# Optimization experiments

Measured on AMD Instinct MI355X. Metric: run time of the kernel, lower is better.

The kernel has to match this reference:

```python
import jax, jax.numpy as jnp
import numpy as np

B, T, D, H, O, E = 2, 2048, 1024, 4096, 1024, 8


def setup_inputs() -> dict:
    key = jax.random.key(0)
    ks = jax.random.split(key, 8)
    s = lambda fan_in: 1.0 / np.sqrt(fan_in)
    return {
        "x": jax.random.normal(ks[0], (B, T, D), dtype=jnp.float32),
        "Wg": jax.random.uniform(ks[1], (D, E), minval=-s(D), maxval=s(D)),
        "bg": jax.random.uniform(ks[2], (E,), minval=-s(D), maxval=s(D)),
        "W1": jax.random.uniform(ks[3], (E, D, H), minval=-s(D), maxval=s(D)),
        "b1": jax.random.uniform(ks[4], (E, H), minval=-s(D), maxval=s(D)),
        "W2": jax.random.uniform(ks[5], (E, H, O), minval=-s(H), maxval=s(H)),
        "b2": jax.random.uniform(ks[6], (E, O), minval=-s(H), maxval=s(H)),
        "num_experts_per_tok": 2,
    }


def reference(x, Wg, bg, W1, b1, W2, b2, num_experts_per_tok):
    # gating: softmax over experts  [B,T,E]
    scores = jax.nn.softmax(jnp.einsum('btd,de->bte', x, Wg) + bg, axis=-1)
    # top-k mask (scatter of ones at topk indices)
    _, idx = jax.lax.top_k(scores, num_experts_per_tok)          # [B,T,k]
    mask = jax.nn.one_hot(idx, E, dtype=scores.dtype).sum(axis=-2)  # [B,T,E]
    gated = scores * mask
    # F.normalize(p=1): divide by L1 norm clamped to eps
    gated = gated / jnp.maximum(jnp.sum(jnp.abs(gated), axis=-1, keepdims=True), 1e-12)
    # all experts run on all tokens (naive MoE)
    hidden = jax.nn.relu(jnp.einsum('btd,edh->beth', x, W1) + b1[None, :, None, :])  # [B,E,T,H]
    expert_out = jnp.einsum('beth,eho->beto', hidden, W2) + b2[None, :, None, :]     # [B,E,T,O]
    # combine: einsum('bte,bteo->bto') with expert_outputs transposed(1,2)
    return jnp.einsum('bte,beto->bto', gated, expert_out)
```

## Files before the change

### kernel.cpp

```cpp
#include <hip/hip_runtime.h>
#include <hip/hip_bf16.h>
#include <cstdio>

#define NT_TOK 4096
#define D_DIM  1024
#define H_DIM  4096
#define O_DIM  1024
#define E_NUM  8
#define PAIRS  8192
#define WI_SLOTS 72
#define BK 64
#define G1_BLOCKS (32 * WI_SLOTS)
#define G2_BLOCKS (8 * WI_SLOTS)
#define TW1_BLOCKS (E_NUM * 1024)
#define TW2_BLOCKS (E_NUM * 1024)

typedef short bf16x8 __attribute__((ext_vector_type(8)));
typedef float f32x4  __attribute__((ext_vector_type(4)));

__device__ __forceinline__ unsigned short bfr(float f){
  unsigned u = __float_as_uint(f);
  unsigned r = (u + 0x7FFFu + ((u >> 16) & 1u)) >> 16;
  return (unsigned short)r;
}

__device__ __forceinline__ void gload_lds16(const void* g, void* l){
  __builtin_amdgcn_global_load_lds((const __attribute__((address_space(1))) unsigned int*)g,
                                   (__attribute__((address_space(3))) unsigned int*)l,
                                   16, 0, 0);
}

__device__ __forceinline__ void transpose_tile(const float* __restrict__ in,
                                               unsigned short* __restrict__ out,
                                               int R, int C, int bx, int by, int bz,
                                               char* smem){
  float (*t)[65] = (float(*)[65])smem;
  long long base = (long long)bz * R * C;
  int c0 = bx * 64, r0 = by * 64;
  int tid = threadIdx.x;
  int rr = tid >> 4;
  int cc = (tid & 15) * 4;
  #pragma unroll
  for (int i = 0; i < 4; i++){
    int r = rr + i * 16;
    float4 v = *(const float4*)&in[base + (long long)(r0 + r) * C + c0 + cc];
    t[r][cc] = v.x; t[r][cc+1] = v.y; t[r][cc+2] = v.z; t[r][cc+3] = v.w;
  }
  __syncthreads();
  #pragma unroll
  for (int i = 0; i < 4; i++){
    int oc = rr + i * 16;
    unsigned int lo = (unsigned int)bfr(t[cc][oc])   | ((unsigned int)bfr(t[cc+1][oc]) << 16);
    unsigned int hi = (unsigned int)bfr(t[cc+2][oc]) | ((unsigned int)bfr(t[cc+3][oc]) << 16);
    *(uint2*)&out[base + (long long)(c0 + oc) * R + r0 + cc] = make_uint2(lo, hi);
  }
}

__global__ __launch_bounds__(256) void gate_w1t_kernel(const float* __restrict__ x,
                                                       const float* __restrict__ Wg,
                                                       const float* __restrict__ bg,
                                                       const float* __restrict__ W1,
                                                       unsigned short* __restrict__ xb,
                                                       unsigned short* __restrict__ W1t,
                                                       int*   __restrict__ pe,
                                                       float* __restrict__ pw,
                                                       int*   __restrict__ chist){
  __shared__ __align__(16) char smem[16640];
  int bid = blockIdx.x;
  if (bid >= NT_TOK/4){
    int tb = bid - NT_TOK/4;
    int e = tb >> 10, t = tb & 1023;
    transpose_tile(W1, W1t, D_DIM, H_DIM, t & 63, t >> 6, e, smem);
    return;
  }
  int wid = threadIdx.x >> 6, lane = threadIdx.x & 63;
  int t = bid * 4 + wid;
  const float* xr = x + (long long)t * D_DIM;
  unsigned short* xo = xb + (long long)t * D_DIM;
  float acc[E_NUM];
  #pragma unroll
  for (int e = 0; e < E_NUM; e++) acc[e] = 0.f;
  for (int d = lane; d < D_DIM; d += 64){
    float xv = xr[d];
    xo[d] = bfr(xv);
    const float* wr = Wg + d * E_NUM;
    #pragma unroll
    for (int e = 0; e < E_NUM; e++) acc[e] += xv * wr[e];
  }
  #pragma unroll
  for (int off = 32; off; off >>= 1)
    #pragma unroll
    for (int e = 0; e < E_NUM; e++) acc[e] += __shfl_xor(acc[e], off);
  if (lane == 0){
    float l[E_NUM];
    float m = -1e30f;
    #pragma unroll
    for (int e = 0; e < E_NUM; e++){ l[e] = acc[e] + bg[e]; m = fmaxf(m, l[e]); }
    float ex[E_NUM];
    #pragma unroll
    for (int e = 0; e < E_NUM; e++) ex[e] = expf(l[e] - m);
    int e0 = 0;
    #pragma unroll
    for (int e = 1; e < E_NUM; e++) if (ex[e] > ex[e0]) e0 = e;
    int e1 = -1;
    for (int e = 0; e < E_NUM; e++){ if (e == e0) continue; if (e1 < 0 || ex[e] > ex[e1]) e1 = e; }
    float s = ex[e0] + ex[e1];
    pe[2*t]   = e0;  pw[2*t]   = ex[e0] / s;
    pe[2*t+1] = e1;  pw[2*t+1] = ex[e1] / s;
    int chunk = (2*t) >> 8;
    atomicAdd(&chist[chunk * E_NUM + e0], 1);
    atomicAdd(&chist[chunk * E_NUM + e1], 1);
  }
}

__global__ __launch_bounds__(256) void scatter_kernel(const int* __restrict__ pe,
                                                      const int* __restrict__ chunk_hist,
                                                      int* __restrict__ cnt,
                                                      int* __restrict__ offs,
                                                      int* __restrict__ row_pair,
                                                      int* __restrict__ wi){
  __shared__ int hist[32][E_NUM];
  __shared__ int pref[32][E_NUM];
  __shared__ int total[E_NUM];
  __shared__ int off_s[E_NUM + 1];
  __shared__ unsigned char ex[PAIRS];
  int tid = threadIdx.x;
  for (int i = tid; i < PAIRS; i += 256) ex[i] = (unsigned char)pe[i];
  { int c = tid >> 3, e = tid & 7; hist[c][e] = chunk_hist[tid]; }
  __syncthreads();
  if (tid < E_NUM){
    int s = 0;
    for (int c = 0; c < 32; c++){ pref[c][tid] = s; s += hist[c][tid]; }
    total[tid] = s;
  }
  __syncthreads();
  if (tid == 0){
    int s = 0;
    for (int e = 0; e < E_NUM; e++){ off_s[e] = s; s += total[e]; }
    off_s[E_NUM] = s;
    int idx = 0;
    for (int e = 0; e < E_NUM; e++){
      int mts = (total[e] + 127) >> 7;
      for (int m = 0; m < mts; m++) wi[idx++] = (e << 8) | m;
    }
    for (; idx < WI_SLOTS; idx++) wi[idx] = -1;
  }
  __syncthreads();
  if (tid < E_NUM){ cnt[tid] = total[tid]; offs[tid] = off_s[tid]; }
  int c = tid >> 3, e = tid & 7;
  int base = off_s[e] + pref[c][e];
  int local = 0;
  for (int i = 0; i < 256; i++){
    int p = c * 256 + i;
    if (ex[p] == (unsigned char)e){
      row_pair[base + local] = p;
      local++;
    }
  }
}

__global__ __launch_bounds__(256, 3) void gemm1_w2t_kernel(const unsigned short* __restrict__ xb,
                                                           const unsigned short* __restrict__ W1t,
                                                           const float* __restrict__ W2,
                                                           unsigned short* __restrict__ W2t,
                                                           const float* __restrict__ b1,
                                                           const int* __restrict__ row_pair,
                                                           const int* __restrict__ cnt,
                                                           const int* __restrict__ offs,
                                                           const int* __restrict__ wi,
                                                           unsigned short* __restrict__ hidden){
  __shared__ __align__(16) char smem[32768];
  int bid = blockIdx.x;
  if (bid >= G1_BLOCKS){
    int tb = bid - G1_BLOCKS;
    int e = tb >> 10, t = tb & 1023;
    transpose_tile(W2, W2t, H_DIM, O_DIM, t & 15, t >> 4, e, smem);
    return;
  }
  int nt = bid & 31, slot = bid >> 5;
  int w = wi[slot];
  if (w < 0) return;
  int e = w >> 8, mt = w & 255;
  int count = cnt[e];
  int m0 = mt * 128;
  int seg = offs[e];
  int valid = count - m0;
  int n0 = nt * 128;

  unsigned short* As = (unsigned short*)smem;
  unsigned short* Bs = (unsigned short*)(smem + 16384);

  int tid = threadIdx.x;
  int wv = tid >> 6, lane = tid & 63;
  int wr = wv >> 1, wc = wv & 1;
  int lo = lane & 15, hi = lane >> 4;
  int l3 = lane >> 3;
  int srcel = ((lane & 7) ^ l3) << 3;

  const unsigned short* w1e = W1t + (long long)e * H_DIM * D_DIM;

  const unsigned short* pa[4];
  const unsigned short* pb[4];
  #pragma unroll
  for (int h = 0; h < 4; h++){
    int r = h * 32 + wv * 8 + l3;
    int pos = seg + m0 + r; if (pos > PAIRS - 1) pos = PAIRS - 1;
    int token = row_pair[pos] >> 1;
    pa[h] = xb + (long long)token * D_DIM + srcel;
    pb[h] = w1e + (long long)(n0 + r) * D_DIM + srcel;
  }

  f32x4 acc[4][4] = {};
  for (int kt = 0; kt < D_DIM / BK; ++kt){
    #pragma unroll
    for (int h = 0; h < 4; h++){
      gload_lds16(pa[h], &As[(h*32 + wv*8) * BK]);  pa[h] += BK;
      gload_lds16(pb[h], &Bs[(h*32 + wv*8) * BK]);  pb[h] += BK;
    }
    __syncthreads();
    bf16x8 aq[4][2], bq[4][2];
    #pragma unroll
    for (int n = 0; n < 4; n++)
      #pragma unroll
      for (int ks = 0; ks < 2; ks++){
        int br = wc*64 + n*16 + lo;
        bq[n][ks] = *(const bf16x8*)&Bs[br*BK + ((ks*32 + hi*8) ^ ((br & 7) << 3))];
      }
    #pragma unroll
    for (int m = 0; m < 4; m++)
      #pragma unroll
      for (int ks = 0; ks < 2; ks++){
        int ar = wr*64 + m*16 + lo;
        aq[m][ks] = *(const bf16x8*)&As[ar*BK + ((ks*32 + hi*8) ^ ((ar & 7) << 3))];
      }
    #pragma unroll
    for (int m = 0; m < 4; m++)
      #pragma unroll
      for (int n = 0; n < 4; n++)
        #pragma unroll
        for (int ks = 0; ks < 2; ks++)
          acc[m][n] = __builtin_amdgcn_mfma_f32_16x16x32_bf16(aq[m][ks], bq[n][ks], acc[m][n], 0, 0, 0);
    __syncthreads();
  }

  const float* b1e = b1 + (long long)e * H_DIM;
  #pragma unroll
  for (int n = 0; n < 4; n++){
    int col = n0 + wc*64 + n*16 + lo;
    float bias = b1e[col];
    #pragma unroll
    for (int m = 0; m < 4; m++)
      #pragma unroll
      for (int j = 0; j < 4; j++){
        int rl = wr*64 + m*16 + hi*4 + j;
        if (rl < valid){
          float v = acc[m][n][j] + bias;
          v = v > 0.f ? v : 0.f;
          hidden[(long long)(seg + m0 + rl) * H_DIM + col] = bfr(v);
        }
      }
  }
}

__global__ __launch_bounds__(256, 3) void gemm2_kernel(const unsigned short* __restrict__ hidden,
                                                       const unsigned short* __restrict__ W2t,
                                                       const float* __restrict__ b2,
                                                       const int* __restrict__ row_pair,
                                                       const int* __restrict__ cnt,
                                                       const int* __restrict__ offs,
                                                       const int* __restrict__ wi,
                                                       float* __restrict__ y){
  int bid = blockIdx.x;
  int fp = (bid & 7) * (G2_BLOCKS / 8) + (bid >> 3);
  int nt = fp & 7, slot = fp >> 3;
  int w = wi[slot];
  if (w < 0) return;
  int e = w >> 8, mt = w & 255;
  int count = cnt[e];
  int m0 = mt * 128;
  int seg = offs[e];
  int valid = count - m0;
  int n0 = nt * 128;

  __shared__ unsigned short As[128 * BK];
  __shared__ unsigned short Bs[128 * BK];

  int tid = threadIdx.x;
  int wv = tid >> 6, lane = tid & 63;
  int wr = wv >> 1, wc = wv & 1;
  int lo = lane & 15, hi = lane >> 4;
  int l3 = lane >> 3;
  int srcel = ((lane & 7) ^ l3) << 3;

  const unsigned short* w2e = W2t + (long long)e * O_DIM * H_DIM;

  const unsigned short* pa[4];
  const unsigned short* pb[4];
  #pragma unroll
  for (int h = 0; h < 4; h++){
    int r = h * 32 + wv * 8 + l3;
    long long pos = seg + m0 + r; if (pos > PAIRS - 1) pos = PAIRS - 1;
    pa[h] = hidden + pos * H_DIM + srcel;
    pb[h] = w2e + (long long)(n0 + r) * H_DIM + srcel;
  }

  f32x4 acc[4][4] = {};
  for (int kt = 0; kt < H_DIM / BK; ++kt){
    #pragma unroll
    for (int h = 0; h < 4; h++){
      gload_lds16(pa[h], &As[(h*32 + wv*8) * BK]);  pa[h] += BK;
      gload_lds16(pb[h], &Bs[(h*32 + wv*8) * BK]);  pb[h] += BK;
    }
    __syncthreads();
    bf16x8 aq[4][2], bq[4][2];
    #pragma unroll
    for (int n = 0; n < 4; n++)
      #pragma unroll
      for (int ks = 0; ks < 2; ks++){
        int br = wc*64 + n*16 + lo;
        bq[n][ks] = *(const bf16x8*)&Bs[br*BK + ((ks*32 + hi*8) ^ ((br & 7) << 3))];
      }
    #pragma unroll
    for (int m = 0; m < 4; m++)
      #pragma unroll
      for (int ks = 0; ks < 2; ks++){
        int ar = wr*64 + m*16 + lo;
        aq[m][ks] = *(const bf16x8*)&As[ar*BK + ((ks*32 + hi*8) ^ ((ar & 7) << 3))];
      }
    #pragma unroll
    for (int m = 0; m < 4; m++)
      #pragma unroll
      for (int n = 0; n < 4; n++)
        #pragma unroll
        for (int ks = 0; ks < 2; ks++)
          acc[m][n] = __builtin_amdgcn_mfma_f32_16x16x32_bf16(aq[m][ks], bq[n][ks], acc[m][n], 0, 0, 0);
    __syncthreads();
  }

  const float* b2e = b2 + (long long)e * O_DIM;
  #pragma unroll
  for (int m = 0; m < 4; m++)
    #pragma unroll
    for (int j = 0; j < 4; j++){
      int rl = wr*64 + m*16 + hi*4 + j;
      if (rl < valid){
        int p = row_pair[seg + m0 + rl];
        float* yr = y + (long long)p * O_DIM;
        #pragma unroll
        for (int n = 0; n < 4; n++){
          int col = n0 + wc*64 + n*16 + lo;
          yr[col] = acc[m][n][j] + b2e[col];
        }
      }
    }
}

__global__ __launch_bounds__(256) void combine_kernel(const float* __restrict__ y,
                                                      const int* __restrict__ pe,
                                                      const float* __restrict__ pw,
                                                      float* __restrict__ out){
  int t = blockIdx.x, tid = threadIdx.x;
  float w0 = pw[2*t], w1 = pw[2*t+1];
  float4 a = ((const float4*)(y + (long long)(2*t) * O_DIM))[tid];
  float4 b = ((const float4*)(y + (long long)(2*t+1) * O_DIM))[tid];
  float4 r;
  r.x = w0 * a.x + w1 * b.x;
  r.y = w0 * a.y + w1 * b.y;
  r.z = w0 * a.z + w1 * b.z;
  r.w = w0 * a.w + w1 * b.w;
  ((float4*)(out + (long long)t * O_DIM))[tid] = r;
}

extern "C" void kernel_launch(void* const* d_in, const int* in_sizes, int n_in,
                              void* d_out, int out_size, void* d_ws, size_t ws_size,
                              hipStream_t stream){
  const float* x  = (const float*)d_in[0];
  const float* Wg = (const float*)d_in[1];
  const float* bg = (const float*)d_in[2];
  const float* W1 = (const float*)d_in[3];
  const float* b1 = (const float*)d_in[4];
  const float* W2 = (const float*)d_in[5];
  const float* b2 = (const float*)d_in[6];
  float* out = (float*)d_out;

  char* ws = (char*)d_ws;
  size_t off = 0;
  auto alloc = [&](size_t bytes){ size_t r = off; off += (bytes + 255) & ~(size_t)255; return r; };

  unsigned short* W1t    = (unsigned short*)(ws + alloc((size_t)E_NUM * H_DIM * D_DIM * 2));
  unsigned short* W2t    = (unsigned short*)(ws + alloc((size_t)E_NUM * O_DIM * H_DIM * 2));
  unsigned short* xb     = (unsigned short*)(ws + alloc((size_t)NT_TOK * D_DIM * 2));
  unsigned short* hidden = (unsigned short*)(ws + alloc((size_t)PAIRS * H_DIM * 2));
  int*            pe     = (int*)           (ws + alloc(PAIRS * 4));
  float*          pw     = (float*)         (ws + alloc(PAIRS * 4));
  int*            row_pair = (int*)         (ws + alloc(PAIRS * 4));
  int*            cnt    = (int*)           (ws + alloc(64));
  int*            offs   = (int*)           (ws + alloc(64));
  int*            chist  = (int*)           (ws + alloc(32 * E_NUM * 4));
  int*            wi     = (int*)           (ws + alloc(WI_SLOTS * 4));

  float* yp = (float*)W1t;

  if (off > ws_size)
    fprintf(stderr, "kernel_launch: workspace too small: need %zu, have %zu\n", off, ws_size);

  hipMemsetAsync(chist, 0, 32 * E_NUM * 4, stream);
  gate_w1t_kernel<<<NT_TOK/4 + TW1_BLOCKS, 256, 0, stream>>>(x, Wg, bg, W1, xb, W1t, pe, pw, chist);
  scatter_kernel<<<1, 256, 0, stream>>>(pe, chist, cnt, offs, row_pair, wi);
  gemm1_w2t_kernel<<<G1_BLOCKS + TW2_BLOCKS, 256, 0, stream>>>(xb, W1t, W2, W2t, b1,
                                                               row_pair, cnt, offs, wi, hidden);
  gemm2_kernel<<<G2_BLOCKS, 256, 0, stream>>>(hidden, W2t, b2, row_pair, cnt, offs, wi, yp);
  combine_kernel<<<NT_TOK, 256, 0, stream>>>(yp, pe, pw, out);
}
```

Measured before the change: 308.8 us.

## Split-K the second expert GEMM and overlap the W1 transpose with scatter

The second GEMM now splits its K dimension (H) into two halves, doubling the block count so more CUs are busy, and writes two partial fp32 outputs that the combine kernel sums before applying gate weights. The W1 transpose moves out of the gating kernel into the scatter kernel's launch, so the single-block scatter runs alongside the transpose blocks instead of as its own serialized launch. The cost is an extra 32 MB partial buffer written and read back, plus one more wave of global traffic in combine.

Result: slower. 350.9 us (+13.6%).

```diff
diff --git a/kernel.cpp b/kernel.cpp
--- a/kernel.cpp
+++ b/kernel.cpp
@@ -11,7 +11,7 @@
 #define WI_SLOTS 72
 #define BK 64
 #define G1_BLOCKS (32 * WI_SLOTS)
-#define G2_BLOCKS (8 * WI_SLOTS)
+#define G2_BLOCKS (2 * 8 * WI_SLOTS)
 #define TW1_BLOCKS (E_NUM * 1024)
 #define TW2_BLOCKS (E_NUM * 1024)
 
@@ -56,25 +56,15 @@
   }
 }
 
-__global__ __launch_bounds__(256) void gate_w1t_kernel(const float* __restrict__ x,
-                                                       const float* __restrict__ Wg,
-                                                       const float* __restrict__ bg,
-                                                       const float* __restrict__ W1,
-                                                       unsigned short* __restrict__ xb,
-                                                       unsigned short* __restrict__ W1t,
-                                                       int*   __restrict__ pe,
-                                                       float* __restrict__ pw,
-                                                       int*   __restrict__ chist){
-  __shared__ __align__(16) char smem[16640];
-  int bid = blockIdx.x;
-  if (bid >= NT_TOK/4){
-    int tb = bid - NT_TOK/4;
-    int e = tb >> 10, t = tb & 1023;
-    transpose_tile(W1, W1t, D_DIM, H_DIM, t & 63, t >> 6, e, smem);
-    return;
-  }
+__global__ __launch_bounds__(256) void gating_kernel(const float* __restrict__ x,
+                                                     const float* __restrict__ Wg,
+                                                     const float* __restrict__ bg,
+                                                     unsigned short* __restrict__ xb,
+                                                     int*   __restrict__ pe,
+                                                     float* __restrict__ pw,
+                                                     int*   __restrict__ chist){
   int wid = threadIdx.x >> 6, lane = threadIdx.x & 63;
-  int t = bid * 4 + wid;
+  int t = blockIdx.x * 4 + wid;
   const float* xr = x + (long long)t * D_DIM;
   unsigned short* xo = xb + (long long)t * D_DIM;
   float acc[E_NUM];
@@ -113,24 +103,34 @@
   }
 }
 
-__global__ __launch_bounds__(256) void scatter_kernel(const int* __restrict__ pe,
-                                                      const int* __restrict__ chunk_hist,
-                                                      int* __restrict__ cnt,
-                                                      int* __restrict__ offs,
-                                                      int* __restrict__ row_pair,
-                                                      int* __restrict__ wi){
-  __shared__ int hist[32][E_NUM];
-  __shared__ int pref[32][E_NUM];
-  __shared__ int total[E_NUM];
-  __shared__ int off_s[E_NUM + 1];
-  __shared__ unsigned char ex[PAIRS];
+__global__ __launch_bounds__(256) void w1t_scatter_kernel(const float* __restrict__ W1,
+                                                          unsigned short* __restrict__ W1t,
+                                                          const int* __restrict__ pe,
+                                                          const int* __restrict__ chunk_hist,
+                                                          int* __restrict__ cnt,
+                                                          int* __restrict__ offs,
+                                                          int* __restrict__ row_pair,
+                                                          int* __restrict__ wi){
+  __shared__ __align__(16) char smem[16640];
+  int bid = blockIdx.x;
+  if (bid > 0){
+    int tb = bid - 1;
+    int e = tb >> 10, t = tb & 1023;
+    transpose_tile(W1, W1t, D_DIM, H_DIM, t & 63, t >> 6, e, smem);
+    return;
+  }
+  int* hist  = (int*)smem;
+  int* pref  = (int*)(smem + 1024);
+  int* total = (int*)(smem + 2048);
+  int* off_s = (int*)(smem + 2084);
+  unsigned char* ex = (unsigned char*)(smem + 2128);
   int tid = threadIdx.x;
   for (int i = tid; i < PAIRS; i += 256) ex[i] = (unsigned char)pe[i];
-  { int c = tid >> 3, e = tid & 7; hist[c][e] = chunk_hist[tid]; }
+  hist[tid] = chunk_hist[tid];
   __syncthreads();
   if (tid < E_NUM){
     int s = 0;
-    for (int c = 0; c < 32; c++){ pref[c][tid] = s; s += hist[c][tid]; }
+    for (int c = 0; c < 32; c++){ pref[c*E_NUM + tid] = s; s += hist[c*E_NUM + tid]; }
     total[tid] = s;
   }
   __syncthreads();
@@ -148,7 +148,7 @@
   __syncthreads();
   if (tid < E_NUM){ cnt[tid] = total[tid]; offs[tid] = off_s[tid]; }
   int c = tid >> 3, e = tid & 7;
-  int base = off_s[e] + pref[c][e];
+  int base = off_s[e] + pref[c*E_NUM + e];
   int local = 0;
   for (int i = 0; i < 256; i++){
     int p = c * 256 + i;
@@ -269,10 +269,14 @@
                                                        const int* __restrict__ cnt,
                                                        const int* __restrict__ offs,
                                                        const int* __restrict__ wi,
-                                                       float* __restrict__ y){
+                                                       float* __restrict__ y0,
+                                                       float* __restrict__ y1){
   int bid = blockIdx.x;
   int fp = (bid & 7) * (G2_BLOCKS / 8) + (bid >> 3);
-  int nt = fp & 7, slot = fp >> 3;
+  int nt = fp & 7;
+  int r2 = fp >> 3;
+  int kpart = r2 / WI_SLOTS;
+  int slot  = r2 % WI_SLOTS;
   int w = wi[slot];
   if (w < 0) return;
   int e = w >> 8, mt = w & 255;
@@ -281,6 +285,8 @@
   int seg = offs[e];
   int valid = count - m0;
   int n0 = nt * 128;
+  int k0 = kpart * (H_DIM / 2);
+  float* y = kpart ? y1 : y0;
 
   __shared__ unsigned short As[128 * BK];
   __shared__ unsigned short Bs[128 * BK];
@@ -300,12 +306,12 @@
   for (int h = 0; h < 4; h++){
     int r = h * 32 + wv * 8 + l3;
     long long pos = seg + m0 + r; if (pos > PAIRS - 1) pos = PAIRS - 1;
-    pa[h] = hidden + pos * H_DIM + srcel;
-    pb[h] = w2e + (long long)(n0 + r) * H_DIM + srcel;
+    pa[h] = hidden + pos * H_DIM + k0 + srcel;
+    pb[h] = w2e + (long long)(n0 + r) * H_DIM + k0 + srcel;
   }
 
   f32x4 acc[4][4] = {};
-  for (int kt = 0; kt < H_DIM / BK; ++kt){
+  for (int kt = 0; kt < (H_DIM / 2) / BK; ++kt){
     #pragma unroll
     for (int h = 0; h < 4; h++){
       gload_lds16(pa[h], &As[(h*32 + wv*8) * BK]);  pa[h] += BK;
@@ -349,25 +355,30 @@
         #pragma unroll
         for (int n = 0; n < 4; n++){
           int col = n0 + wc*64 + n*16 + lo;
-          yr[col] = acc[m][n][j] + b2e[col];
+          float v = acc[m][n][j];
+          if (kpart == 0) v += b2e[col];
+          yr[col] = v;
         }
       }
     }
 }
 
-__global__ __launch_bounds__(256) void combine_kernel(const float* __restrict__ y,
+__global__ __launch_bounds__(256) void combine_kernel(const float* __restrict__ y0,
+                                                      const float* __restrict__ y1,
                                                       const int* __restrict__ pe,
                                                       const float* __restrict__ pw,
                                                       float* __restrict__ out){
   int t = blockIdx.x, tid = threadIdx.x;
   float w0 = pw[2*t], w1 = pw[2*t+1];
-  float4 a = ((const float4*)(y + (long long)(2*t) * O_DIM))[tid];
-  float4 b = ((const float4*)(y + (long long)(2*t+1) * O_DIM))[tid];
+  float4 a0 = ((const float4*)(y0 + (long long)(2*t) * O_DIM))[tid];
+  float4 a1 = ((const float4*)(y1 + (long long)(2*t) * O_DIM))[tid];
+  float4 b0 = ((const float4*)(y0 + (long long)(2*t+1) * O_DIM))[tid];
+  float4 b1 = ((const float4*)(y1 + (long long)(2*t+1) * O_DIM))[tid];
   float4 r;
-  r.x = w0 * a.x + w1 * b.x;
-  r.y = w0 * a.y + w1 * b.y;
-  r.z = w0 * a.z + w1 * b.z;
-  r.w = w0 * a.w + w1 * b.w;
+  r.x = w0 * (a0.x + a1.x) + w1 * (b0.x + b1.x);
+  r.y = w0 * (a0.y + a1.y) + w1 * (b0.y + b1.y);
+  r.z = w0 * (a0.z + a1.z) + w1 * (b0.z + b1.z);
+  r.w = w0 * (a0.w + a1.w) + w1 * (b0.w + b1.w);
   ((float4*)(out + (long long)t * O_DIM))[tid] = r;
 }
 
@@ -391,6 +402,7 @@
   unsigned short* W2t    = (unsigned short*)(ws + alloc((size_t)E_NUM * O_DIM * H_DIM * 2));
   unsigned short* xb     = (unsigned short*)(ws + alloc((size_t)NT_TOK * D_DIM * 2));
   unsigned short* hidden = (unsigned short*)(ws + alloc((size_t)PAIRS * H_DIM * 2));
+  float*          y1     = (float*)         (ws + alloc((size_t)PAIRS * O_DIM * 4));
   int*            pe     = (int*)           (ws + alloc(PAIRS * 4));
   float*          pw     = (float*)         (ws + alloc(PAIRS * 4));
   int*            row_pair = (int*)         (ws + alloc(PAIRS * 4));
@@ -399,16 +411,16 @@
   int*            chist  = (int*)           (ws + alloc(32 * E_NUM * 4));
   int*            wi     = (int*)           (ws + alloc(WI_SLOTS * 4));
 
-  float* yp = (float*)W1t;
+  float* y0 = (float*)W1t;
 
   if (off > ws_size)
     fprintf(stderr, "kernel_launch: workspace too small: need %zu, have %zu\n", off, ws_size);
 
   hipMemsetAsync(chist, 0, 32 * E_NUM * 4, stream);
-  gate_w1t_kernel<<<NT_TOK/4 + TW1_BLOCKS, 256, 0, stream>>>(x, Wg, bg, W1, xb, W1t, pe, pw, chist);
-  scatter_kernel<<<1, 256, 0, stream>>>(pe, chist, cnt, offs, row_pair, wi);
+  gating_kernel<<<NT_TOK/4, 256, 0, stream>>>(x, Wg, bg, xb, pe, pw, chist);
+  w1t_scatter_kernel<<<1 + TW1_BLOCKS, 256, 0, stream>>>(W1, W1t, pe, chist, cnt, offs, row_pair, wi);
   gemm1_w2t_kernel<<<G1_BLOCKS + TW2_BLOCKS, 256, 0, stream>>>(xb, W1t, W2, W2t, b1,
                                                                row_pair, cnt, offs, wi, hidden);
-  gemm2_kernel<<<G2_BLOCKS, 256, 0, stream>>>(hidden, W2t, b2, row_pair, cnt, offs, wi, yp);
-  combine_kernel<<<NT_TOK, 256, 0, stream>>>(yp, pe, pw, out);
-}
+  gemm2_kernel<<<G2_BLOCKS, 256, 0, stream>>>(hidden, W2t, b2, row_pair, cnt, offs, wi, y0, y1);
+  combine_kernel<<<NT_TOK, 256, 0, stream>>>(y0, y1, pe, pw, out);
+}
```
